# Kernel tuning notes

Measured on AMD Instinct MI355X. Metric: run time of the kernel, lower is better.

The kernel has to match this reference:

```python
import jax, jax.numpy as jnp
import numpy as np

T_TOK, N_UNITS, E, H, L_PATH, N_PATHS, B, VOCAB = 16, 4096, 128, 128, 32, 1024, 8, 16384
MAX_PATH_LEN = 32
PAD_ID = 0


def _run_lstm(x, Wi, Wh, b):
    # x: [T, N, E]; torch gate order i, f, g, o
    Hh = Wh.shape[1]
    h0 = jnp.zeros((x.shape[1], Hh), x.dtype)
    def step(carry, xt):
        h, c = carry
        g = xt @ Wi.T + h @ Wh.T + b
        i, f, gg, o = jnp.split(g, 4, axis=-1)
        c = jax.nn.sigmoid(f) * c + jax.nn.sigmoid(i) * jnp.tanh(gg)
        h = jax.nn.sigmoid(o) * jnp.tanh(c)
        return (h, c), h
    _, ys = jax.lax.scan(step, (h0, h0), x)
    return ys


def _bilstm(x, lengths, Wif, Whf, bf, Wib, Whb, bb):
    # emulates pack_padded_sequence + bidirectional LSTM + pad_packed (zeros past length)
    T = x.shape[0]
    t = jnp.arange(T)[:, None]
    valid = t < lengths[None, :]
    out_f = _run_lstm(x, Wif, Whf, bf)
    rev = jnp.clip(lengths[None, :] - 1 - t, 0, T - 1)  # reverse within each valid prefix
    x_rev = jnp.take_along_axis(x, rev[:, :, None], axis=0)
    out_b = jnp.take_along_axis(_run_lstm(x_rev, Wib, Whb, bb), rev[:, :, None], axis=0)
    return jnp.concatenate([out_f, out_b], axis=-1) * valid[:, :, None]


def _layernorm(x, g, b):
    m = x.mean(-1, keepdims=True)
    v = ((x - m) ** 2).mean(-1, keepdims=True)
    return (x - m) * jax.lax.rsqrt(v + 1e-5) * g + b


def _forward(units, paths, unit_per_data, path_per_data, emb, tl_Wif, tl_Whf, tl_bf,
             tl_Wib, tl_Whb, tl_bb, lin_W, lin_b, ln_g, ln_b, attn_w, attn_b,
             pl_Wif, pl_Whf, pl_bf, pl_Wib, pl_Whb, pl_bb, ul_W, ul_b):
    # ---- _token_encoder ----
    is_pad = units == PAD_ID
    tok_len = jnp.where(is_pad.any(0), jnp.argmax(is_pad, 0), units.shape[0])
    x = emb[units]                                              # [T, NU, E]
    h = _bilstm(x, tok_len, tl_Wif, tl_Whf, tl_bf, tl_Wib, tl_Whb, tl_bb)  # [T, NU, 2H]
    out = h @ lin_W.T + lin_b                                   # [T, NU, E]
    q = jnp.tanh(_layernorm(out, ln_g, ln_b))
    scores = q @ attn_w.T + attn_b                              # [T, NU, 1] local attention
    scores = jnp.where(is_pad[:, :, None], -1e9, scores)
    w = jax.nn.softmax(scores, axis=0)
    tok_feat = jnp.einsum('tn,tne->ne', w[..., 0], out)         # [NU, E]
    # ---- _unit_to_path (vectorized ragged gather) ----
    Lp, Pn = paths.shape
    has_end = (paths == -1).any(0)
    fe = jnp.where(has_end, jnp.argmax(paths == -1, 0), Lp)
    ML = min(Lp, MAX_PATH_LEN)
    nb = unit_per_data.shape[0]
    data_of_path = jnp.repeat(jnp.arange(nb), path_per_data, total_repeat_length=Pn)
    u_off = jnp.cumsum(unit_per_data) - unit_per_data
    off_p = u_off[data_of_path]
    un_p = unit_per_data[data_of_path]
    pL = paths[:ML]
    t = jnp.arange(ML)[:, None]
    within = t < fe[None, :]
    keep = within & (pL >= 0) & (pL < un_p[None, :])
    gidx = jnp.clip(jnp.clip(pL, 0, None) + off_p[None, :], 0, tok_feat.shape[0] - 1)
    feats = tok_feat[gidx] * keep[:, :, None]                   # [ML, P, E]
    mask = jnp.where(within, (pL < 0) | (pL > un_p[None, :]), True)
    # ---- _path_encoder ----
    p_len = jnp.where(mask.any(0), jnp.argmax(mask, 0), ML)
    hp = _bilstm(feats, p_len, pl_Wif, pl_Whf, pl_bf, pl_Wib, pl_Whb, pl_bb)
    return hp @ ul_W.T + ul_b                                   # [ML, P, E]


def setup_inputs() -> dict:
    rng = np.random.default_rng(0)
    tok_len = rng.integers(4, T_TOK + 1, N_UNITS); tok_len[0] = T_TOK
    units = rng.integers(1, VOCAB, (T_TOK, N_UNITS))
    units = np.where(np.arange(T_TOK)[:, None] < tok_len[None, :], units, PAD_ID)
    upd = N_UNITS // B
    p_len = rng.integers(8, L_PATH + 1, N_PATHS); p_len[0] = L_PATH
    paths = rng.integers(0, upd, (L_PATH, N_PATHS))
    paths = np.where(np.arange(L_PATH)[:, None] < p_len[None, :], paths, -1)
    key = jax.random.key(0)
    ks = iter(jax.random.split(key, 24))
    def pn(shape, s=0.08):
        return (jax.random.normal(next(ks), shape) * s).astype(jnp.float32)
    return dict(
        units=jnp.asarray(units, jnp.int32),
        paths=jnp.asarray(paths, jnp.int32),
        unit_per_data=jnp.full((B,), upd, jnp.int32),
        path_per_data=jnp.full((B,), N_PATHS // B, jnp.int32),
        emb=pn((VOCAB, E)),
        tl_Wif=pn((4 * H, E)), tl_Whf=pn((4 * H, H)), tl_bf=pn((4 * H,)),
        tl_Wib=pn((4 * H, E)), tl_Whb=pn((4 * H, H)), tl_bb=pn((4 * H,)),
        lin_W=pn((E, 2 * H)), lin_b=pn((E,)),
        ln_g=jnp.ones((E,), jnp.float32), ln_b=jnp.zeros((E,), jnp.float32),
        attn_w=pn((1, E)), attn_b=pn((1,)),
        pl_Wif=pn((4 * H, E)), pl_Whf=pn((4 * H, H)), pl_bf=pn((4 * H,)),
        pl_Wib=pn((4 * H, E)), pl_Whb=pn((4 * H, H)), pl_bb=pn((4 * H,)),
        ul_W=pn((E, 2 * H)), ul_b=pn((E,)),
    )


def reference(units, paths, unit_per_data, path_per_data, emb, tl_Wif, tl_Whf, tl_bf,
              tl_Wib, tl_Whb, tl_bb, lin_W, lin_b, ln_g, ln_b, attn_w, attn_b,
              pl_Wif, pl_Whf, pl_bf, pl_Wib, pl_Whb, pl_bb, ul_W, ul_b):
    return _forward(units, paths, unit_per_data, path_per_data, emb, tl_Wif, tl_Whf, tl_bf,
                    tl_Wib, tl_Whb, tl_bb, lin_W, lin_b, ln_g, ln_b, attn_w, attn_b,
                    pl_Wif, pl_Whf, pl_bf, pl_Wib, pl_Whb, pl_bb, ul_W, ul_b)
```

## Files before the change

kernel.cpp:

```cpp
#include <hip/hip_runtime.h>
#include <cstdint>
#include <cstddef>

#define T_TOKN 16
#define NUNITS 4096
#define LPATH  32
#define NPATHS 1024
#define BNUM   8

typedef __attribute__((ext_vector_type(8))) short short8;
typedef __attribute__((ext_vector_type(4))) float f32x4;

enum : size_t {
  OFF_WFRAG   = 0,
  OFF_LINFRAG = 262144,
  OFF_OUTF    = 294912,
  OFF_OUTB    = OFF_OUTF + 4194304,
  OFF_OUTLIN  = OFF_OUTB + 4194304,
  OFF_SCORES  = OFF_OUTLIN + 8388608,
  OFF_TOKFEAT = OFF_SCORES + 65536,
  OFF_POUTF   = OFF_TOKFEAT + 524288,
  OFF_POUTB   = OFF_POUTF + 2097152,
  OFF_INT     = OFF_POUTB + 2097152,
  WS_FLOATS   = OFF_INT + 8192
};

static __device__ __forceinline__ unsigned short f2bf(float f) {
  union { float f; unsigned u; } v; v.f = f;
  unsigned r = v.u + 0x7fffu + ((v.u >> 16) & 1u);
  return (unsigned short)(r >> 16);
}
static __device__ __forceinline__ unsigned pack_bf(float a, float b) {
  return (unsigned)f2bf(a) | ((unsigned)f2bf(b) << 16);
}
static __device__ __forceinline__ float sigf(float x)      { return 1.f / (1.f + __expf(-x)); }
static __device__ __forceinline__ float tanhfast(float x)  { return 2.f / (1.f + __expf(-2.f * x)) - 1.f; }

__global__ void prep_kernel(
    const float* __restrict__ tWif, const float* __restrict__ tWhf,
    const float* __restrict__ tWib, const float* __restrict__ tWhb,
    const float* __restrict__ pWif, const float* __restrict__ pWhf,
    const float* __restrict__ pWib, const float* __restrict__ pWhb,
    const float* __restrict__ linW, const float* __restrict__ ulW,
    const int* __restrict__ units, const int* __restrict__ paths,
    const int* __restrict__ upd, const int* __restrict__ ppd,
    float* __restrict__ ws, int* __restrict__ ip)
{
  int idx = blockIdx.x * 256 + threadIdx.x;
  if (idx < 524288) {
    unsigned short* wf = (unsigned short*)(ws + OFF_WFRAG);
    int mat = idx >> 17, rem = idx & 131071;
    int i  = rem & 7;
    int lane = (rem >> 3) & 63;
    int ct = (rem >> 9) & 3;
    int ks = (rem >> 11) & 7;
    int wv = (rem >> 14) & 7;
    int g = wv * 64 + ct * 16 + (lane & 15);
    int k = ks * 32 + ((lane >> 4) << 3) + i;
    const float* Wi; const float* Wh;
    switch (mat) {
      case 0: Wi = tWif; Wh = tWhf; break;
      case 1: Wi = tWib; Wh = tWhb; break;
      case 2: Wi = pWif; Wh = pWhf; break;
      default: Wi = pWib; Wh = pWhb; break;
    }
    float v = (k < 128) ? Wi[g * 128 + k] : Wh[g * 128 + (k - 128)];
    wf[idx] = f2bf(v);
  } else if (idx < 524288 + 65536) {
    unsigned short* lf = (unsigned short*)(ws + OFF_LINFRAG);
    int i2 = idx - 524288;
    int mat = i2 >> 15, rem = i2 & 32767;
    int i  = rem & 7;
    int lane = (rem >> 3) & 63;
    int ks = (rem >> 9) & 7;
    int ct = (rem >> 12) & 7;
    int e = ct * 16 + (lane & 15);
    int k = ks * 32 + ((lane >> 4) << 3) + i;
    const float* W = mat ? ulW : linW;
    lf[i2] = f2bf(W[e * 256 + k]);
  } else if (idx < 589824 + 4096) {
    int n = idx - 589824;
    int len = T_TOKN;
    for (int t = 0; t < T_TOKN; ++t)
      if (units[t * NUNITS + n] == 0) { len = t; break; }
    ip[n] = len;
  } else if (idx < 589824 + 5120) {
    int p = idx - (589824 + 4096);
    int* fe_a  = ip + 4096;
    int* p_len = ip + 5120;
    int* off_p = ip + 6144;
    int* un_p  = ip + 7168;
    int cum = 0; int d = BNUM - 1;
    for (int dd = 0; dd < BNUM; ++dd) {
      int c2 = cum + ppd[dd];
      if (p < c2) { d = dd; break; }
      cum = c2;
    }
    int off = 0;
    for (int dd = 0; dd < d; ++dd) off += upd[dd];
    int un = upd[d];
    off_p[p] = off; un_p[p] = un;
    int f = LPATH;
    for (int t = 0; t < LPATH; ++t)
      if (paths[t * NPATHS + p] == -1) { f = t; break; }
    fe_a[p] = f;
    int pl = LPATH;
    for (int t = 0; t < LPATH; ++t) {
      int v = paths[t * NPATHS + p];
      if ((t >= f) || (v < 0) || (v > un)) { pl = t; break; }
    }
    p_len[p] = pl;
  }
}

template <int MODE>
__global__ __launch_bounds__(1024, 4) void lstm_kernel(
    const unsigned short* __restrict__ wfragAll,
    const float* __restrict__ biasF, const float* __restrict__ biasB,
    const float* __restrict__ src,
    const int* __restrict__ idxsrc,
    const int* __restrict__ lens,
    const int* __restrict__ fe_a, const int* __restrict__ off_p, const int* __restrict__ un_p,
    unsigned short* __restrict__ outF, unsigned short* __restrict__ outB)
{
  constexpr int NN   = MODE ? NPATHS : NUNITS;
  constexpr int TT   = MODE ? LPATH : T_TOKN;
  constexpr int GR   = MODE ? 4 : 16;
  constexpr int ASTR = 264;
  constexpr int GSTR = 514;

  __shared__ unsigned short ash[2][16 * ASTR];
  __shared__ float gates[2][16 * GSTR];

  int tid  = threadIdx.x;
  int dir  = blockIdx.y;
  int n0   = blockIdx.x * (2 * GR);
  int lane = tid & 63, wv = tid >> 6;
  int koq  = (lane >> 4) << 3;

  const unsigned short* wbase =
      wfragAll + (size_t)((MODE ? 2 : 0) + dir) * 131072;
  int wv8 = wv >> 1;
  short8 bfr[8][2];
#pragma unroll
  for (int ks = 0; ks < 8; ++ks)
#pragma unroll
    for (int c2 = 0; c2 < 2; ++c2) {
      int ct = ((wv & 1) << 1) | c2;
      bfr[ks][c2] = *(const short8*)&wbase[((((wv8 * 8 + ks) * 4 + ct) * 64) + lane) * 8];
    }

  for (int i = tid; i < 2 * 16 * ASTR / 2; i += 1024) ((unsigned*)ash)[i] = 0u;

  int j2 = MODE ? (tid & 127) : (lane * 2);
  int ug = MODE ? (tid >> 7) : (tid >> 6);

  int nn[2], ulen[2];
  int gfe[2] = {0, 0}, goff[2] = {0, 0}, gun[2] = {0, 0};
#pragma unroll
  for (int g = 0; g < 2; ++g) {
    int n = n0 + g * GR + ug;
    if constexpr (MODE) n = min(n, NPATHS - 1);
    nn[g] = n; ulen[g] = lens[n];
    if constexpr (MODE) { gfe[g] = fe_a[n]; goff[g] = off_p[n]; gun[g] = un_p[n]; }
  }

  const float* bcp = dir ? biasB : biasF;
  float2 b2[4];
#pragma unroll
  for (int q = 0; q < 4; ++q) {
    if constexpr (MODE == 0) b2[q] = *(const float2*)&bcp[q * 128 + j2];
    else                     b2[q] = make_float2(bcp[q * 128 + j2], 0.f);
  }

  float cst0[2] = {0.f, 0.f}, cst1[2] = {0.f, 0.f};
  float2 xq2[2];
  float  xq1[2];
  (void)xq2; (void)xq1; (void)cst1;

#define XLOAD(GG, TN) do {                                                    \
    int tc = min((TN), TT - 1);                                               \
    if constexpr (MODE == 0) {                                                \
      int tau = dir ? min(max(ulen[GG] - 1 - tc, 0), TT - 1) : tc;            \
      int tok = idxsrc[tau * NN + nn[GG]];                                    \
      xq2[GG] = *(const float2*)&src[(size_t)tok * 128 + j2];                 \
    } else {                                                                  \
      if (ug < GR) {                                                          \
        int tau = dir ? min(max(ulen[GG] - 1 - tc, 0), TT - 1) : tc;          \
        int v = idxsrc[tau * NN + nn[GG]];                                    \
        bool keep = (tau < gfe[GG]) && (v >= 0) && (v < gun[GG]);             \
        float xv = 0.f;                                                       \
        if (keep) xv = src[(size_t)min(v + goff[GG], NUNITS - 1) * 128 + j2]; \
        xq1[GG] = xv;                                                         \
      }                                                                       \
    }                                                                         \
  } while (0)

#define XWRITE(GG) do {                                                       \
    if constexpr (MODE == 0)                                                  \
      *(unsigned*)&ash[GG][ug * ASTR + j2] = pack_bf(xq2[GG].x, xq2[GG].y);   \
    else if (ug < GR)                                                         \
      ash[GG][ug * ASTR + j2] = f2bf(xq1[GG]);                                \
  } while (0)

#define GSTORE(GG, P0, P1) do {                                               \
    int col = wv * 32 + (lane & 15);                                          \
    int ub  = (lane >> 4) << 2;                                               \
    float* gg = gates[GG];                                                    \
    for (int r = 0; r < 4; ++r) {                                             \
      gg[(ub + r) * GSTR + col]      = (P0)[r];                               \
      gg[(ub + r) * GSTR + col + 16] = (P1)[r];                               \
    }                                                                         \
  } while (0)

#define POINTWISE(GG, TPW) do {                                               \
    int tpw = (TPW);                                                          \
    if constexpr (MODE == 0) {                                                \
      int L = ulen[GG]; int n = nn[GG];                                       \
      if (tpw < L) {                                 \
        const float* gg = gates[GG] + ug * GSTR + j2;                         \
        float2 g0 = *(const float2*)(gg);                                     \
        float2 g1 = *(const float2*)(gg + 128);                               \
        float2 g2 = *(const float2*)(gg + 256);                               \
        float2 g3 = *(const float2*)(gg + 384);                               \
        float i0 = sigf(g0.x + b2[0].x), i1 = sigf(g0.y + b2[0].y);           \
        float f0 = sigf(g1.x + b2[1].x), f1 = sigf(g1.y + b2[1].y);           \
        float c0 = tanhfast(g2.x + b2[2].x), c1 = tanhfast(g2.y + b2[2].y);   \
        float o0 = sigf(g3.x + b2[3].x), o1 = sigf(g3.y + b2[3].y);           \
        float cA = f0 * cst0[GG] + i0 * c0;                                   \
        float cB = f1 * cst1[GG] + i1 * c1;                                   \
        cst0[GG] = cA; cst1[GG] = cB;                                         \
        unsigned hp = pack_bf(o0 * tanhfast(cA), o1 * tanhfast(cB));          \
        *(unsigned*)&ash[GG][ug * ASTR + 128 + j2] = hp;                      \
        if (dir == 0)                                                         \
          *(unsigned*)&outF[((size_t)tpw * NN + n) * 128 + j2] = hp;          \
        else                                                                  \
          *(unsigned*)&outB[((size_t)(L - 1 - tpw) * NN + n) * 128 + j2] = hp;\
      } else {                 \
        if (dir == 0)                                                         \
          *(unsigned*)&outF[((size_t)tpw * NN + n) * 128 + j2] = 0u;          \
        else                                                                  \
          *(unsigned*)&outB[((size_t)tpw * NN + n) * 128 + j2] = 0u;          \
      }                                                                       \
    } else if (ug < GR) {                                                     \
      int L = ulen[GG]; int n = nn[GG];                                       \
      if (tpw < L) {                                                          \
        const float* gg = gates[GG] + ug * GSTR + j2;                         \
        float p0 = gg[0]   + b2[0].x;                                         \
        float p1 = gg[128] + b2[1].x;                                         \
        float p2 = gg[256] + b2[2].x;                                         \
        float p3 = gg[384] + b2[3].x;                                         \
        float c = sigf(p1) * cst0[GG] + sigf(p0) * tanhfast(p2);              \
        cst0[GG] = c;                                                         \
        unsigned short hb = f2bf(sigf(p3) * tanhfast(c));                     \
        ash[GG][ug * ASTR + 128 + j2] = hb;                                   \
        if (dir == 0) outF[((size_t)tpw * NN + n) * 128 + j2] = hb;           \
        else          outB[((size_t)(L - 1 - tpw) * NN + n) * 128 + j2] = hb; \
      } else {                                                                \
        if (dir == 0) outF[((size_t)tpw * NN + n) * 128 + j2] = 0;            \
        else          outB[((size_t)tpw * NN + n) * 128 + j2] = 0;            \
      }                                                                       \
    }                                                                         \
  } while (0)

  __syncthreads();
  XLOAD(0, 0);
  XLOAD(1, 0);
  XWRITE(0);
  __syncthreads();

#pragma unroll 1
  for (int t = 0; t < TT; ++t) {
    {
      f32x4 p0 = {0.f, 0.f, 0.f, 0.f}, p1 = {0.f, 0.f, 0.f, 0.f};
#pragma unroll
      for (int ks = 0; ks < 8; ++ks) {
        short8 a = *(const short8*)&ash[0][(lane & 15) * ASTR + ks * 32 + koq];
        p0 = __builtin_amdgcn_mfma_f32_16x16x32_bf16(a, bfr[ks][0], p0, 0, 0, 0);
        p1 = __builtin_amdgcn_mfma_f32_16x16x32_bf16(a, bfr[ks][1], p1, 0, 0, 0);
      }
      XWRITE(1);
      if (t + 1 < TT) XLOAD(0, t + 1);
      if (t > 0) POINTWISE(1, t - 1);
      GSTORE(0, p0, p1);
    }
    __syncthreads();

    {
      f32x4 p0 = {0.f, 0.f, 0.f, 0.f}, p1 = {0.f, 0.f, 0.f, 0.f};
#pragma unroll
      for (int ks = 0; ks < 8; ++ks) {
        short8 a = *(const short8*)&ash[1][(lane & 15) * ASTR + ks * 32 + koq];
        p0 = __builtin_amdgcn_mfma_f32_16x16x32_bf16(a, bfr[ks][0], p0, 0, 0, 0);
        p1 = __builtin_amdgcn_mfma_f32_16x16x32_bf16(a, bfr[ks][1], p1, 0, 0, 0);
      }
      if (t + 1 < TT) XWRITE(0);
      if (t + 1 < TT) XLOAD(1, t + 1);
      POINTWISE(0, t);
      GSTORE(1, p0, p1);
    }
    __syncthreads();
  }
  POINTWISE(1, TT - 1);

#undef XLOAD
#undef XWRITE
#undef GSTORE
#undef POINTWISE
}

template <int EPI>
__global__ __launch_bounds__(256) void gemm_mfma(
    const unsigned short* __restrict__ INf, const unsigned short* __restrict__ INb,
    const int* __restrict__ lens,
    const unsigned short* __restrict__ Bfrag, const float* __restrict__ bias,
    float* __restrict__ OUT, float* __restrict__ scores,
    const float* __restrict__ lng, const float* __restrict__ lnb,
    const float* __restrict__ attw, const float* __restrict__ attb,
    const int* __restrict__ units, int Nn)
{
  constexpr int OSTR = 132;
  __shared__ float outs[64 * OSTR];
  __shared__ float red1[256];
  __shared__ float red2[256];
  __shared__ float rowm[64], rowr[64];
  __shared__ float awsh[128], lgsh[128], lbsh[128];

  int tid = threadIdx.x, lane = tid & 63, wv = tid >> 6;
  int row0 = blockIdx.x * 64;
  int t = row0 / Nn, n0 = row0 % Nn;

  if (EPI == 1 && tid < 128) {
    awsh[tid] = attw[tid]; lgsh[tid] = lng[tid]; lbsh[tid] = lnb[tid];
  }

  short8 bfr[8][2];
#pragma unroll
  for (int ks = 0; ks < 8; ++ks)
#pragma unroll
    for (int c2 = 0; c2 < 2; ++c2) {
      int ct = wv * 2 + c2;
      bfr[ks][c2] = *(const short8*)&Bfrag[(((ct * 8 + ks) * 64) + lane) * 8];
    }

  int rb = lane & 15;
  int koq = (lane >> 4) << 3;
  bool val[4];
#pragma unroll
  for (int rt = 0; rt < 4; ++rt)
    val[rt] = (EPI == 1) ? true : (t < lens[n0 + rt * 16 + rb]);

  f32x4 acc[4][2];
#pragma unroll
  for (int rt = 0; rt < 4; ++rt)
#pragma unroll
    for (int c2 = 0; c2 < 2; ++c2) {
      f32x4 z = {0.f, 0.f, 0.f, 0.f};
      acc[rt][c2] = z;
    }

#pragma unroll
  for (int ks = 0; ks < 8; ++ks) {
    const unsigned short* P = (ks < 4) ? INf : INb;
    int koff = (ks & 3) * 32 + koq;
#pragma unroll
    for (int rt = 0; rt < 4; ++rt) {
      short8 a = {0, 0, 0, 0, 0, 0, 0, 0};
      if (val[rt])
        a = *(const short8*)&P[((size_t)(row0 + rt * 16 + rb)) * 128 + koff];
#pragma unroll
      for (int c2 = 0; c2 < 2; ++c2)
        acc[rt][c2] = __builtin_amdgcn_mfma_f32_16x16x32_bf16(
            a, bfr[ks][c2], acc[rt][c2], 0, 0, 0);
    }
  }

  float bc[2];
#pragma unroll
  for (int c2 = 0; c2 < 2; ++c2) bc[c2] = bias[wv * 32 + c2 * 16 + rb];
#pragma unroll
  for (int rt = 0; rt < 4; ++rt)
#pragma unroll
    for (int c2 = 0; c2 < 2; ++c2) {
      int col = wv * 32 + c2 * 16 + rb;
      int ub  = rt * 16 + ((lane >> 4) << 2);
#pragma unroll
      for (int r = 0; r < 4; ++r)
        outs[(ub + r) * OSTR + col] = acc[rt][c2][r] + bc[c2];
    }
  __syncthreads();

  int row = tid >> 2, seg = tid & 3;
  const float* rp = &outs[row * OSTR + seg * 32];
  size_t go = ((size_t)(row0 + row)) * 128 + seg * 32;

  if (EPI == 0) {
#pragma unroll
    for (int x = 0; x < 8; ++x)
      *(f32x4*)&OUT[go + x * 4] = *(const f32x4*)&rp[x * 4];
  } else {
    f32x4 v[8];
    float s = 0.f, s2 = 0.f;
#pragma unroll
    for (int x = 0; x < 8; ++x) {
      v[x] = *(const f32x4*)&rp[x * 4];
#pragma unroll
      for (int c = 0; c < 4; ++c) { s += v[x][c]; s2 += v[x][c] * v[x][c]; }
    }
    red1[tid] = s; red2[tid] = s2;
    __syncthreads();
    if (tid < 64) {
      float a = red1[tid * 4] + red1[tid * 4 + 1] + red1[tid * 4 + 2] + red1[tid * 4 + 3];
      float b = red2[tid * 4] + red2[tid * 4 + 1] + red2[tid * 4 + 2] + red2[tid * 4 + 3];
      float m = a * (1.f / 128.f);
      float var = b * (1.f / 128.f) - m * m;
      rowm[tid] = m;
      rowr[tid] = rsqrtf(var + 1e-5f);
    }
    __syncthreads();
    float m = rowm[row], rs = rowr[row];
    float sp = 0.f;
#pragma unroll
    for (int x = 0; x < 8; ++x) {
#pragma unroll
      for (int c = 0; c < 4; ++c) {
        int col = seg * 32 + x * 4 + c;
        float q = tanhfast((v[x][c] - m) * rs * lgsh[col] + lbsh[col]);
        sp += q * awsh[col];
      }
      *(f32x4*)&OUT[go + x * 4] = v[x];
    }
    red1[tid] = sp;
    __syncthreads();
    if (tid < 64) {
      float s3 = red1[tid * 4] + red1[tid * 4 + 1] + red1[tid * 4 + 2] + red1[tid * 4 + 3]
               + attb[0];
      int n = n0 + tid;
      if (units[t * NUNITS + n] == 0) s3 = -1e9f;
      scores[t * NUNITS + n] = s3;
    }
  }
}

__global__ __launch_bounds__(128) void softmax_feat_kernel(
    const float* __restrict__ scores, const float* __restrict__ out_lin,
    float* __restrict__ tok_feat)
{
  int n = blockIdx.x;
  int e = threadIdx.x;
  float s[T_TOKN];
  float m = -1e30f;
#pragma unroll
  for (int t = 0; t < T_TOKN; ++t) { s[t] = scores[t * NUNITS + n]; m = fmaxf(m, s[t]); }
  float sum = 0.f;
#pragma unroll
  for (int t = 0; t < T_TOKN; ++t) { s[t] = expf(s[t] - m); sum += s[t]; }
  float inv = 1.f / sum;
  float a = 0.f;
#pragma unroll
  for (int t = 0; t < T_TOKN; ++t)
    a += s[t] * inv * out_lin[((size_t)t * NUNITS + n) * 128 + e];
  tok_feat[n * 128 + e] = a;
}

extern "C" void kernel_launch(void* const* d_in, const int* in_sizes, int n_in,
                              void* d_out, int out_size, void* d_ws, size_t ws_size,
                              hipStream_t stream)
{
  const int*   units = (const int*)d_in[0];
  const int*   paths = (const int*)d_in[1];
  const int*   upd   = (const int*)d_in[2];
  const int*   ppd   = (const int*)d_in[3];
  const float* emb   = (const float*)d_in[4];
  const float* tWif  = (const float*)d_in[5];
  const float* tWhf  = (const float*)d_in[6];
  const float* tbf   = (const float*)d_in[7];
  const float* tWib  = (const float*)d_in[8];
  const float* tWhb  = (const float*)d_in[9];
  const float* tbb   = (const float*)d_in[10];
  const float* linW  = (const float*)d_in[11];
  const float* linb  = (const float*)d_in[12];
  const float* lng   = (const float*)d_in[13];
  const float* lnb   = (const float*)d_in[14];
  const float* attw  = (const float*)d_in[15];
  const float* attb  = (const float*)d_in[16];
  const float* pWif  = (const float*)d_in[17];
  const float* pWhf  = (const float*)d_in[18];
  const float* pbf   = (const float*)d_in[19];
  const float* pWib  = (const float*)d_in[20];
  const float* pWhb  = (const float*)d_in[21];
  const float* pbb   = (const float*)d_in[22];
  const float* ulW   = (const float*)d_in[23];
  const float* ulb   = (const float*)d_in[24];

  float* ws = (float*)d_ws;
  int*   ip = (int*)(ws + OFF_INT);
  if (ws_size < WS_FLOATS * sizeof(float)) return;

  unsigned short* wfrag   = (unsigned short*)(ws + OFF_WFRAG);
  unsigned short* linfrag = (unsigned short*)(ws + OFF_LINFRAG);
  unsigned short* ulfrag  = linfrag + 32768;
  unsigned short* OUTF  = (unsigned short*)(ws + OFF_OUTF);
  unsigned short* OUTB  = (unsigned short*)(ws + OFF_OUTB);
  unsigned short* POUTF = (unsigned short*)(ws + OFF_POUTF);
  unsigned short* POUTB = (unsigned short*)(ws + OFF_POUTB);

  prep_kernel<<<2324, 256, 0, stream>>>(tWif, tWhf, tWib, tWhb,
                                        pWif, pWhf, pWib, pWhb,
                                        linW, ulW, units, paths, upd, ppd,
                                        ws, ip);

  lstm_kernel<0><<<dim3(128, 2), 1024, 0, stream>>>(
      wfrag, tbf, tbb, emb, units, ip , nullptr, nullptr, nullptr,
      OUTF, OUTB);

  gemm_mfma<1><<<1024, 256, 0, stream>>>(
      OUTF, OUTB, ip , linfrag, linb,
      ws + OFF_OUTLIN, ws + OFF_SCORES, lng, lnb, attw, attb, units, NUNITS);

  softmax_feat_kernel<<<4096, 128, 0, stream>>>(ws + OFF_SCORES, ws + OFF_OUTLIN,
                                                ws + OFF_TOKFEAT);

  lstm_kernel<1><<<dim3(128, 2), 1024, 0, stream>>>(
      wfrag, pbf, pbb, ws + OFF_TOKFEAT, paths, ip + 5120 ,
      ip + 4096 , ip + 6144 , ip + 7168 ,
      POUTF, POUTB);

  gemm_mfma<0><<<512, 256, 0, stream>>>(
      POUTF, POUTB, ip + 5120 , ulfrag, ulb,
      (float*)d_out, nullptr, nullptr, nullptr, nullptr, nullptr, nullptr, NPATHS);
}
```

Baseline: 330.7 us.

## Reorder LSTM weight fragments so each wave owns all four gates, dropping gate shared buffer

The LSTM weight fragments are re-laid out so each of 8 waves holds i/f/g/o columns for the same 16 hidden units. The pointwise cell update can then run directly on MFMA accumulators, with no round trip through a shared-memory gate buffer. Block size drops from 1024 to 512 threads, and the path LSTM now packs 32 paths per block instead of 8, cutting its grid from 128 to 32 blocks. Per-thread register use rises (32 B-fragments plus 8 accumulators), and the path LSTM runs far fewer blocks.

```diff
diff --git a/kernel.cpp b/kernel.cpp
--- a/kernel.cpp
+++ b/kernel.cpp
@@ -9,6 +9,7 @@
 #define BNUM   8
 
 typedef __attribute__((ext_vector_type(8))) short short8;
+typedef __attribute__((ext_vector_type(4))) short short4x;
 typedef __attribute__((ext_vector_type(4))) float f32x4;
 
 enum : size_t {
@@ -29,9 +30,6 @@
   union { float f; unsigned u; } v; v.f = f;
   unsigned r = v.u + 0x7fffu + ((v.u >> 16) & 1u);
   return (unsigned short)(r >> 16);
-}
-static __device__ __forceinline__ unsigned pack_bf(float a, float b) {
-  return (unsigned)f2bf(a) | ((unsigned)f2bf(b) << 16);
 }
 static __device__ __forceinline__ float sigf(float x)      { return 1.f / (1.f + __expf(-x)); }
 static __device__ __forceinline__ float tanhfast(float x)  { return 2.f / (1.f + __expf(-2.f * x)) - 1.f; }
@@ -50,12 +48,12 @@
   if (idx < 524288) {
     unsigned short* wf = (unsigned short*)(ws + OFF_WFRAG);
     int mat = idx >> 17, rem = idx & 131071;
-    int i  = rem & 7;
+    int i    = rem & 7;
     int lane = (rem >> 3) & 63;
-    int ct = (rem >> 9) & 3;
-    int ks = (rem >> 11) & 7;
-    int wv = (rem >> 14) & 7;
-    int g = wv * 64 + ct * 16 + (lane & 15);
+    int ks   = (rem >> 9) & 7;
+    int q    = (rem >> 12) & 3;
+    int w    = (rem >> 14) & 7;
+    int g = q * 128 + w * 16 + (lane & 15);
     int k = ks * 32 + ((lane >> 4) << 3) + i;
     const float* Wi; const float* Wh;
     switch (mat) {
@@ -114,7 +112,7 @@
 }
 
 template <int MODE>
-__global__ __launch_bounds__(1024, 4) void lstm_kernel(
+__global__ __launch_bounds__(512, 2) void lstm_kernel(
     const unsigned short* __restrict__ wfragAll,
     const float* __restrict__ biasF, const float* __restrict__ biasB,
     const float* __restrict__ src,
@@ -125,188 +123,140 @@
 {
   constexpr int NN   = MODE ? NPATHS : NUNITS;
   constexpr int TT   = MODE ? LPATH : T_TOKN;
-  constexpr int GR   = MODE ? 4 : 16;
   constexpr int ASTR = 264;
-  constexpr int GSTR = 514;
-
-  __shared__ unsigned short ash[2][16 * ASTR];
-  __shared__ float gates[2][16 * GSTR];
-
-  int tid  = threadIdx.x;
-  int dir  = blockIdx.y;
-  int n0   = blockIdx.x * (2 * GR);
-  int lane = tid & 63, wv = tid >> 6;
-  int koq  = (lane >> 4) << 3;
+
+  __shared__ __align__(16) unsigned short ash[2][16 * ASTR];
+
+  const int tid  = threadIdx.x;
+  const int dir  = blockIdx.y;
+  const int n0   = blockIdx.x * 32;
+  const int lane = tid & 63, wv = tid >> 6;
+  const int cl   = lane & 15, quad = lane >> 4;
+  const int koq  = quad << 3;
+  const int jj   = wv * 16 + cl;
 
   const unsigned short* wbase =
       wfragAll + (size_t)((MODE ? 2 : 0) + dir) * 131072;
-  int wv8 = wv >> 1;
-  short8 bfr[8][2];
+  short8 bfr[8][4];
 #pragma unroll
   for (int ks = 0; ks < 8; ++ks)
 #pragma unroll
-    for (int c2 = 0; c2 < 2; ++c2) {
-      int ct = ((wv & 1) << 1) | c2;
-      bfr[ks][c2] = *(const short8*)&wbase[((((wv8 * 8 + ks) * 4 + ct) * 64) + lane) * 8];
-    }
-
-  for (int i = tid; i < 2 * 16 * ASTR / 2; i += 1024) ((unsigned*)ash)[i] = 0u;
-
-  int j2 = MODE ? (tid & 127) : (lane * 2);
-  int ug = MODE ? (tid >> 7) : (tid >> 6);
-
-  int nn[2], ulen[2];
-  int gfe[2] = {0, 0}, goff[2] = {0, 0}, gun[2] = {0, 0};
-#pragma unroll
-  for (int g = 0; g < 2; ++g) {
-    int n = n0 + g * GR + ug;
-    if constexpr (MODE) n = min(n, NPATHS - 1);
-    nn[g] = n; ulen[g] = lens[n];
-    if constexpr (MODE) { gfe[g] = fe_a[n]; goff[g] = off_p[n]; gun[g] = un_p[n]; }
-  }
+    for (int q = 0; q < 4; ++q)
+      bfr[ks][q] = *(const short8*)&wbase[(((wv * 4 + q) * 8 + ks) * 64 + lane) * 8];
 
   const float* bcp = dir ? biasB : biasF;
-  float2 b2[4];
-#pragma unroll
-  for (int q = 0; q < 4; ++q) {
-    if constexpr (MODE == 0) b2[q] = *(const float2*)&bcp[q * 128 + j2];
-    else                     b2[q] = make_float2(bcp[q * 128 + j2], 0.f);
-  }
-
-  float cst0[2] = {0.f, 0.f}, cst1[2] = {0.f, 0.f};
-  float2 xq2[2];
-  float  xq1[2];
-  (void)xq2; (void)xq1; (void)cst1;
-
-#define XLOAD(GG, TN) do {                                                    \
-    int tc = min((TN), TT - 1);                                               \
+  float bq[4];
+#pragma unroll
+  for (int q = 0; q < 4; ++q) bq[q] = bcp[q * 128 + jj];
+
+  float cs0[4], cs1[4];
+  int   pl0[4], pl1[4];
+#pragma unroll
+  for (int r = 0; r < 4; ++r) {
+    cs0[r] = 0.f; cs1[r] = 0.f;
+    pl0[r] = lens[n0 + quad * 4 + r];
+    pl1[r] = lens[n0 + 16 + quad * 4 + r];
+  }
+
+  const int grow = tid >> 5;
+  const int gc0  = (tid & 31) * 4;
+  const int gn0 = n0 + grow, gn1 = n0 + 16 + grow;
+  const int glen0 = lens[gn0], glen1 = lens[gn1];
+  int gfe0 = 0, goff0 = 0, gun0 = 0, gfe1 = 0, goff1 = 0, gun1 = 0;
+  if constexpr (MODE) {
+    gfe0 = fe_a[gn0]; goff0 = off_p[gn0]; gun0 = un_p[gn0];
+    gfe1 = fe_a[gn1]; goff1 = off_p[gn1]; gun1 = un_p[gn1];
+  }
+  float4 xq0, xq1;
+
+#define XLOAD(G, XQ, TN) do {                                                 \
+    int tc = (TN); if (tc > TT - 1) tc = TT - 1;                              \
+    int tau = dir ? min(max(glen##G - 1 - tc, 0), TT - 1) : tc;               \
     if constexpr (MODE == 0) {                                                \
-      int tau = dir ? min(max(ulen[GG] - 1 - tc, 0), TT - 1) : tc;            \
-      int tok = idxsrc[tau * NN + nn[GG]];                                    \
-      xq2[GG] = *(const float2*)&src[(size_t)tok * 128 + j2];                 \
+      int tok = idxsrc[tau * NN + gn##G];                                     \
+      XQ = *(const float4*)&src[(size_t)tok * 128 + gc0];                     \
     } else {                                                                  \
-      if (ug < GR) {                                                          \
-        int tau = dir ? min(max(ulen[GG] - 1 - tc, 0), TT - 1) : tc;          \
-        int v = idxsrc[tau * NN + nn[GG]];                                    \
-        bool keep = (tau < gfe[GG]) && (v >= 0) && (v < gun[GG]);             \
-        float xv = 0.f;                                                       \
-        if (keep) xv = src[(size_t)min(v + goff[GG], NUNITS - 1) * 128 + j2]; \
-        xq1[GG] = xv;                                                         \
+      int v = idxsrc[tau * NN + gn##G];                                       \
+      bool keep = (tau < gfe##G) && (v >= 0) && (v < gun##G);                 \
+      if (keep)                                                               \
+        XQ = *(const float4*)&src[(size_t)min(v + goff##G, NUNITS - 1) * 128 + gc0]; \
+      else { XQ.x = 0.f; XQ.y = 0.f; XQ.z = 0.f; XQ.w = 0.f; }                \
+    }                                                                         \
+  } while (0)
+
+#define XWRITE(G, XQ) do {                                                    \
+    short4x xv;                                                               \
+    xv[0] = (short)f2bf(XQ.x); xv[1] = (short)f2bf(XQ.y);                     \
+    xv[2] = (short)f2bf(XQ.z); xv[3] = (short)f2bf(XQ.w);                     \
+    *(short4x*)&ash[G][grow * ASTR + gc0] = xv;                               \
+  } while (0)
+
+#define MFMA_G(G, ACC) do {                                                   \
+    _Pragma("unroll")                                                         \
+    for (int q = 0; q < 4; ++q) { f32x4 z = {0.f, 0.f, 0.f, 0.f}; ACC[q] = z; } \
+    _Pragma("unroll")                                                         \
+    for (int ks = 0; ks < 8; ++ks) {                                          \
+      short8 afr = *(const short8*)&ash[G][cl * ASTR + ks * 32 + koq];        \
+      ACC[0] = __builtin_amdgcn_mfma_f32_16x16x32_bf16(afr, bfr[ks][0], ACC[0], 0, 0, 0); \
+      ACC[1] = __builtin_amdgcn_mfma_f32_16x16x32_bf16(afr, bfr[ks][1], ACC[1], 0, 0, 0); \
+      ACC[2] = __builtin_amdgcn_mfma_f32_16x16x32_bf16(afr, bfr[ks][2], ACC[2], 0, 0, 0); \
+      ACC[3] = __builtin_amdgcn_mfma_f32_16x16x32_bf16(afr, bfr[ks][3], ACC[3], 0, 0, 0); \
+    }                                                                         \
+  } while (0)
+
+#define PW(G, ACC, CST, PLEN, TPW) do {                                       \
+    int tpw = (TPW);                                                          \
+    _Pragma("unroll")                                                         \
+    for (int r = 0; r < 4; ++r) {                                             \
+      float iv = sigf(ACC[0][r] + bq[0]);                                     \
+      float fv = sigf(ACC[1][r] + bq[1]);                                     \
+      float gv = tanhfast(ACC[2][r] + bq[2]);                                 \
+      float ov = sigf(ACC[3][r] + bq[3]);                                     \
+      float c = fv * CST[r] + iv * gv;                                        \
+      CST[r] = c;                                                             \
+      unsigned short hb = f2bf(ov * tanhfast(c));                             \
+      int u = quad * 4 + r;                                                   \
+      ash[G][u * ASTR + 128 + jj] = hb;    \
+      int L = PLEN[r];                                                        \
+      int n = n0 + (G) * 16 + u;                                              \
+      bool vld = tpw < L;                                                     \
+      if (dir == 0) {                                                         \
+        outF[((size_t)tpw * NN + n) * 128 + jj] = vld ? hb : (unsigned short)0; \
+      } else {                                                                \
+        size_t tr = vld ? (size_t)(L - 1 - tpw) : (size_t)tpw;                \
+        outB[(tr * NN + n) * 128 + jj] = vld ? hb : (unsigned short)0;        \
       }                                                                       \
     }                                                                         \
   } while (0)
 
-#define XWRITE(GG) do {                                                       \
-    if constexpr (MODE == 0)                                                  \
-      *(unsigned*)&ash[GG][ug * ASTR + j2] = pack_bf(xq2[GG].x, xq2[GG].y);   \
-    else if (ug < GR)                                                         \
-      ash[GG][ug * ASTR + j2] = f2bf(xq1[GG]);                                \
-  } while (0)
-
-#define GSTORE(GG, P0, P1) do {                                               \
-    int col = wv * 32 + (lane & 15);                                          \
-    int ub  = (lane >> 4) << 2;                                               \
-    float* gg = gates[GG];                                                    \
-    for (int r = 0; r < 4; ++r) {                                             \
-      gg[(ub + r) * GSTR + col]      = (P0)[r];                               \
-      gg[(ub + r) * GSTR + col + 16] = (P1)[r];                               \
-    }                                                                         \
-  } while (0)
-
-#define POINTWISE(GG, TPW) do {                                               \
-    int tpw = (TPW);                                                          \
-    if constexpr (MODE == 0) {                                                \
-      int L = ulen[GG]; int n = nn[GG];                                       \
-      if (tpw < L) {                                 \
-        const float* gg = gates[GG] + ug * GSTR + j2;                         \
-        float2 g0 = *(const float2*)(gg);                                     \
-        float2 g1 = *(const float2*)(gg + 128);                               \
-        float2 g2 = *(const float2*)(gg + 256);                               \
-        float2 g3 = *(const float2*)(gg + 384);                               \
-        float i0 = sigf(g0.x + b2[0].x), i1 = sigf(g0.y + b2[0].y);           \
-        float f0 = sigf(g1.x + b2[1].x), f1 = sigf(g1.y + b2[1].y);           \
-        float c0 = tanhfast(g2.x + b2[2].x), c1 = tanhfast(g2.y + b2[2].y);   \
-        float o0 = sigf(g3.x + b2[3].x), o1 = sigf(g3.y + b2[3].y);           \
-        float cA = f0 * cst0[GG] + i0 * c0;                                   \
-        float cB = f1 * cst1[GG] + i1 * c1;                                   \
-        cst0[GG] = cA; cst1[GG] = cB;                                         \
-        unsigned hp = pack_bf(o0 * tanhfast(cA), o1 * tanhfast(cB));          \
-        *(unsigned*)&ash[GG][ug * ASTR + 128 + j2] = hp;                      \
-        if (dir == 0)                                                         \
-          *(unsigned*)&outF[((size_t)tpw * NN + n) * 128 + j2] = hp;          \
-        else                                                                  \
-          *(unsigned*)&outB[((size_t)(L - 1 - tpw) * NN + n) * 128 + j2] = hp;\
-      } else {                 \
-        if (dir == 0)                                                         \
-          *(unsigned*)&outF[((size_t)tpw * NN + n) * 128 + j2] = 0u;          \
-        else                                                                  \
-          *(unsigned*)&outB[((size_t)tpw * NN + n) * 128 + j2] = 0u;          \
-      }                                                                       \
-    } else if (ug < GR) {                                                     \
-      int L = ulen[GG]; int n = nn[GG];                                       \
-      if (tpw < L) {                                                          \
-        const float* gg = gates[GG] + ug * GSTR + j2;                         \
-        float p0 = gg[0]   + b2[0].x;                                         \
-        float p1 = gg[128] + b2[1].x;                                         \
-        float p2 = gg[256] + b2[2].x;                                         \
-        float p3 = gg[384] + b2[3].x;                                         \
-        float c = sigf(p1) * cst0[GG] + sigf(p0) * tanhfast(p2);              \
-        cst0[GG] = c;                                                         \
-        unsigned short hb = f2bf(sigf(p3) * tanhfast(c));                     \
-        ash[GG][ug * ASTR + 128 + j2] = hb;                                   \
-        if (dir == 0) outF[((size_t)tpw * NN + n) * 128 + j2] = hb;           \
-        else          outB[((size_t)(L - 1 - tpw) * NN + n) * 128 + j2] = hb; \
-      } else {                                                                \
-        if (dir == 0) outF[((size_t)tpw * NN + n) * 128 + j2] = 0;            \
-        else          outB[((size_t)tpw * NN + n) * 128 + j2] = 0;            \
-      }                                                                       \
-    }                                                                         \
-  } while (0)
-
+  for (int i = tid; i < 2 * 16 * ASTR / 2; i += 512) ((unsigned*)ash)[i] = 0u;
+  XLOAD(0, xq0, 0);
+  XLOAD(1, xq1, 0);
   __syncthreads();
-  XLOAD(0, 0);
-  XLOAD(1, 0);
-  XWRITE(0);
+  XWRITE(0, xq0);
   __syncthreads();
+
+  f32x4 acc0[4], acc1[4];
 
 #pragma unroll 1
   for (int t = 0; t < TT; ++t) {
-    {
-      f32x4 p0 = {0.f, 0.f, 0.f, 0.f}, p1 = {0.f, 0.f, 0.f, 0.f};
-#pragma unroll
-      for (int ks = 0; ks < 8; ++ks) {
-        short8 a = *(const short8*)&ash[0][(lane & 15) * ASTR + ks * 32 + koq];
-        p0 = __builtin_amdgcn_mfma_f32_16x16x32_bf16(a, bfr[ks][0], p0, 0, 0, 0);
-        p1 = __builtin_amdgcn_mfma_f32_16x16x32_bf16(a, bfr[ks][1], p1, 0, 0, 0);
-      }
-      XWRITE(1);
-      if (t + 1 < TT) XLOAD(0, t + 1);
-      if (t > 0) POINTWISE(1, t - 1);
-      GSTORE(0, p0, p1);
-    }
+    MFMA_G(0, acc0);
+    if (t > 0) PW(1, acc1, cs1, pl1, t - 1);
+    XWRITE(1, xq1);
+    if (t + 1 < TT) XLOAD(0, xq0, t + 1);
     __syncthreads();
 
-    {
-      f32x4 p0 = {0.f, 0.f, 0.f, 0.f}, p1 = {0.f, 0.f, 0.f, 0.f};
-#pragma unroll
-      for (int ks = 0; ks < 8; ++ks) {
-        short8 a = *(const short8*)&ash[1][(lane & 15) * ASTR + ks * 32 + koq];
-        p0 = __builtin_amdgcn_mfma_f32_16x16x32_bf16(a, bfr[ks][0], p0, 0, 0, 0);
-        p1 = __builtin_amdgcn_mfma_f32_16x16x32_bf16(a, bfr[ks][1], p1, 0, 0, 0);
-      }
-      if (t + 1 < TT) XWRITE(0);
-      if (t + 1 < TT) XLOAD(1, t + 1);
-      POINTWISE(0, t);
-      GSTORE(1, p0, p1);
-    }
+    MFMA_G(1, acc1);
+    PW(0, acc0, cs0, pl0, t);
+    if (t + 1 < TT) { XWRITE(0, xq0); XLOAD(1, xq1, t + 1); }
     __syncthreads();
   }
-  POINTWISE(1, TT - 1);
+  PW(1, acc1, cs1, pl1, TT - 1);
 
 #undef XLOAD
 #undef XWRITE
-#undef GSTORE
-#undef POINTWISE
+#undef MFMA_G
+#undef PW
 }
 
 template <int EPI>
@@ -510,7 +460,7 @@
                                         linW, ulW, units, paths, upd, ppd,
                                         ws, ip);
 
-  lstm_kernel<0><<<dim3(128, 2), 1024, 0, stream>>>(
+  lstm_kernel<0><<<dim3(128, 2), 512, 0, stream>>>(
       wfrag, tbf, tbb, emb, units, ip , nullptr, nullptr, nullptr,
       OUTF, OUTB);
 
@@ -521,7 +471,7 @@
   softmax_feat_kernel<<<4096, 128, 0, stream>>>(ws + OFF_SCORES, ws + OFF_OUTLIN,
                                                 ws + OFF_TOKFEAT);
 
-  lstm_kernel<1><<<dim3(128, 2), 1024, 0, stream>>>(
+  lstm_kernel<1><<<dim3(32, 2), 512, 0, stream>>>(
       wfrag, pbf, pbb, ws + OFF_TOKFEAT, paths, ip + 5120 ,
       ip + 4096 , ip + 6144 , ip + 7168 ,
       POUTF, POUTB);
```

New measurement: 404.0 us. 1.22x slower.
